# Optimization experiments

Measured on AMD Instinct MI355X. Metric: run time of the kernel, lower is better.

## Reference

```python
import jax, jax.numpy as jnp
import numpy as np

B, T, D = 4, 4096, 1024
H = 16
DH = D // H
F = 4096
EPS = 1e-5


def _layernorm(x, gamma, beta):
    mu = jnp.mean(x, axis=-1, keepdims=True)
    var = jnp.var(x, axis=-1, keepdims=True)
    return (x - mu) * jax.lax.rsqrt(var + EPS) * gamma + beta


def setup_inputs() -> dict:
    key = jax.random.key(0)
    ks = jax.random.split(key, 10)
    s = 0.02
    return {
        "x": jax.random.normal(ks[0], (B, T, D), dtype=jnp.float32),
        "Wqkv": jax.random.normal(ks[1], (D, 3 * D), dtype=jnp.float32) * s,
        "bqkv": jnp.zeros((3 * D,), dtype=jnp.float32),
        "Wo": jax.random.normal(ks[2], (D, D), dtype=jnp.float32) * s,
        "bo": jnp.zeros((D,), dtype=jnp.float32),
        "W1": jax.random.normal(ks[3], (D, F), dtype=jnp.float32) * s,
        "b1": jnp.zeros((F,), dtype=jnp.float32),
        "W2": jax.random.normal(ks[4], (F, D), dtype=jnp.float32) * s,
        "b2": jnp.zeros((D,), dtype=jnp.float32),
        "g1": jnp.ones((D,), dtype=jnp.float32),
        "be1": jnp.zeros((D,), dtype=jnp.float32),
        "g2": jnp.ones((D,), dtype=jnp.float32),
        "be2": jnp.zeros((D,), dtype=jnp.float32),
    }


def reference(x, Wqkv, bqkv, Wo, bo, W1, b1, W2, b2, g1, be1, g2, be2):
    # fused QKV projection: [B,T,3D]
    qkv = jnp.einsum("btd,de->bte", x, Wqkv) + bqkv
    q, k, v = jnp.split(qkv, 3, axis=-1)
    # [B,H,T,DH]
    q = q.reshape(B, T, H, DH).transpose(0, 2, 1, 3)
    k = k.reshape(B, T, H, DH).transpose(0, 2, 1, 3)
    v = v.reshape(B, T, H, DH).transpose(0, 2, 1, 3)
    scores = jnp.einsum("bhqd,bhkd->bhqk", q, k) / jnp.sqrt(jnp.float32(DH))
    attn = jax.nn.softmax(scores, axis=-1)
    ctx = jnp.einsum("bhqk,bhkd->bhqd", attn, v)
    ctx = ctx.transpose(0, 2, 1, 3).reshape(B, T, D)
    # output projection + residual + post-LN
    x = _layernorm(x + (jnp.einsum("btd,de->bte", ctx, Wo) + bo), g1, be1)
    # FFN (exact GELU, torch default) + residual + post-LN
    h = jax.nn.gelu(jnp.einsum("btd,df->btf", x, W1) + b1, approximate=False)
    ffn = jnp.einsum("btf,fd->btd", h, W2) + b2
    return _layernorm(x + ffn, g2, be2)
```

## Files before the change

### kernel.cpp

```cpp
#include <hip/hip_runtime.h>
#include <math.h>

typedef unsigned short u16;
typedef unsigned int   u32;
typedef __attribute__((ext_vector_type(8))) short short8;
typedef __attribute__((ext_vector_type(4))) float f32x4;

#define B_  4
#define T_  4096
#define D_  1024
#define H_  16
#define DH_ 64
#define F_  4096
#define EPS_ 1e-5f
#define QKV_LD (3 * D_)

#define QSCALE_ 0.18033688011112042f

__device__ __forceinline__ float b2f(u16 v) {
    union { u32 u; float f; } x; x.u = ((u32)v) << 16; return x.f;
}
__device__ __forceinline__ u16 f2b(float f) {
    union { u32 u; float f; } x; x.f = f;
    u32 r = (x.u >> 16) & 1u;
    return (u16)((x.u + 0x7fffu + r) >> 16);
}

__device__ __forceinline__ float ex2(float x) {
    float r;
    asm("v_exp_f32 %0, %1" : "=v"(r) : "v"(x));
    return r;
}
__device__ __forceinline__ float rcp_(float x) {
    float r;
    asm("v_rcp_f32 %0, %1" : "=v"(r) : "v"(x));
    return r;
}
__device__ __forceinline__ u32 cvtpk(float lo, float hi) {
    u32 r;
    asm("v_cvt_pk_bf16_f32 %0, %1, %2" : "=v"(r) : "v"(lo), "v"(hi));
    return r;
}
template<int CTRL>
__device__ __forceinline__ u32 dppu(u32 v) {
    return (u32)__builtin_amdgcn_update_dpp(0, (int)v, CTRL, 0xF, 0xF, true);
}

__device__ __forceinline__ float gelu_erf(float x) {
    const float z = fabsf(x) * 0.70710678118654752f;
    const float t = rcp_(1.0f + 0.3275911f * z);
    float poly = 1.061405429f;
    poly = poly * t - 1.453152027f;
    poly = poly * t + 1.421413741f;
    poly = poly * t - 0.284496736f;
    poly = poly * t + 0.254829592f;
    poly = poly * t;
    const float e = ex2(-z * z * 1.4426950408889634f);
    const float erfz = 1.0f - poly * e;
    const float se = copysignf(erfz, x);
    return 0.5f * x * (1.0f + se);
}

__device__ __forceinline__ void gll16(const u16* g, u16* ldsbase) {
    __builtin_amdgcn_global_load_lds(
        (const __attribute__((address_space(1))) void*)g,
        (__attribute__((address_space(3))) void*)ldsbase, 16, 0, 0);
}

__global__ __launch_bounds__(256) void conv_bf16_kernel(
    const float* __restrict__ in, u16* __restrict__ out)
{
    const int i = blockIdx.x * 256 + threadIdx.x;
    float4 v = ((const float4*)in)[i];
    ushort4 o;
    o.x = f2b(v.x); o.y = f2b(v.y); o.z = f2b(v.z); o.w = f2b(v.w);
    ((ushort4*)out)[i] = o;
}

__global__ __launch_bounds__(256) void transpose_bf16_kernel(
    const float* __restrict__ W, u16* __restrict__ Wt, int R, int C)
{
    __shared__ float tile[32][33];
    const int bx = blockIdx.x * 32;
    const int by = blockIdx.y * 32;
    const int tx = threadIdx.x & 31, ty = threadIdx.x >> 5;
#pragma unroll
    for (int p = 0; p < 4; ++p)
        tile[ty + p * 8][tx] = W[(size_t)(by + ty + p * 8) * C + bx + tx];
    __syncthreads();
#pragma unroll
    for (int p = 0; p < 4; ++p)
        Wt[(size_t)(bx + ty + p * 8) * R + by + tx] = f2b(tile[tx][ty + p * 8]);
}

template<bool CBF, int KU>
__global__ __launch_bounds__(256) void mfma_gemm(
    const u16* __restrict__ A, int lda,
    const u16* __restrict__ Bt, int ldbt,
    const float* __restrict__ bias,
    void* __restrict__ Cv, int ldc,
    int K, int act, int acc, int qcols)
{
    __shared__ __align__(16) u16 Al[KU][128 * 32];
    __shared__ __align__(16) u16 Bl[KU][128 * 32];

    const int tid  = threadIdx.x;
    const int lane = tid & 63, wave = tid >> 6;
    const int quad = lane >> 4, l16 = lane & 15;

    const int gx = gridDim.x;
    const int nwg = gx * gridDim.y;
    const int lin = blockIdx.y * gx + blockIdx.x;
    const int wg  = (lin & 7) * (nwg >> 3) + (lin >> 3);
    const int m0 = (wg / gx) * 128, n0 = (wg % gx) * 128;

    const int wm = (wave >> 1) * 64, wn = (wave & 1) * 64;

    int srow[2], sgk[2];
#pragma unroll
    for (int t = 0; t < 2; ++t) {
        const int c = wave * 128 + t * 64 + lane;
        srow[t] = c >> 2;
        sgk[t] = ((c & 3) ^ ((srow[t] >> 1) & 3)) * 8;
    }
    const u16* Ag = A  + (size_t)m0 * lda;
    const u16* Bg = Bt + (size_t)n0 * ldbt;
    const int apos = (quad ^ ((l16 >> 1) & 3)) * 8;

    f32x4 accr[4][4];
#pragma unroll
    for (int i = 0; i < 4; ++i)
#pragma unroll
        for (int j = 0; j < 4; ++j)
            accr[i][j] = (f32x4)(0.0f);

    for (int k0 = 0; k0 < K; k0 += 32 * KU) {
        __syncthreads();
#pragma unroll
        for (int h = 0; h < KU; ++h)
#pragma unroll
            for (int t = 0; t < 2; ++t) {
                gll16(Ag + (size_t)srow[t] * lda  + k0 + h * 32 + sgk[t],
                      &Al[h][(wave * 128 + t * 64) * 8]);
                gll16(Bg + (size_t)srow[t] * ldbt + k0 + h * 32 + sgk[t],
                      &Bl[h][(wave * 128 + t * 64) * 8]);
            }
        __syncthreads();

#pragma unroll
        for (int h = 0; h < KU; ++h) {
            short8 af[4], bf[4];
#pragma unroll
            for (int i = 0; i < 4; ++i)
                af[i] = *(const short8*)&Al[h][(wm + i * 16 + l16) * 32 + apos];
#pragma unroll
            for (int j = 0; j < 4; ++j)
                bf[j] = *(const short8*)&Bl[h][(wn + j * 16 + l16) * 32 + apos];
#pragma unroll
            for (int i = 0; i < 4; ++i)
#pragma unroll
                for (int j = 0; j < 4; ++j)
                    accr[i][j] = __builtin_amdgcn_mfma_f32_16x16x32_bf16(
                        af[i], bf[j], accr[i][j], 0, 0, 0);
        }
    }

#pragma unroll
    for (int j = 0; j < 4; ++j) {
        const int cc = n0 + wn + j * 16 + l16;
        float bv = acc ? 0.0f : bias[cc];
        const float sc = (cc < qcols) ? QSCALE_ : 1.0f;
#pragma unroll
        for (int i = 0; i < 4; ++i) {
#pragma unroll
            for (int r = 0; r < 4; ++r) {
                const int rr = m0 + wm + i * 16 + quad * 4 + r;
                float v = (accr[i][j][r] + bv) * sc;
                if (act == 1)
                    v = gelu_erf(v);
                if (CBF) {
                    ((u16*)Cv)[(size_t)rr * ldc + cc] = f2b(v);
                } else {
                    float* dst = (float*)Cv + (size_t)rr * ldc + cc;
                    if (acc) v += *dst;
                    *dst = v;
                }
            }
        }
    }
}

__global__ __launch_bounds__(256) void attn_mfma_kernel(
    const u16* __restrict__ qkv, u16* __restrict__ ctx)
{
    __shared__ u16 Ks[64 * 72];
    __shared__ u16 Vt[64 * 72];
    __shared__ u16 Ps[4][32 * 72];

    const int tid  = threadIdx.x;
    const int lane = tid & 63, wave = tid >> 6;
    const int quad = lane >> 4, l16 = lane & 15;
    const int odd  = l16 & 1;

    const int gx = gridDim.x, gy = gridDim.y;
    const int nwg = gx * gy * gridDim.z;
    const int lin = (blockIdx.z * gy + blockIdx.y) * gx + blockIdx.x;
    const int wg  = (lin & 7) * (nwg >> 3) + (lin >> 3);
    const int q0 = (wg % gx) * 128;
    const int h  = (wg / gx) % gy;
    const int b  = wg / (gx * gy);

    short8 ones8;
#pragma unroll
    for (int i = 0; i < 8; ++i) ones8[i] = (short)0x3F80;

    short8 aq[2][2];
    {
        const u16* qb = qkv + (size_t)(b * T_ + q0 + wave * 32) * QKV_LD + h * DH_;
#pragma unroll
        for (int u = 0; u < 2; ++u)
#pragma unroll
            for (int s = 0; s < 2; ++s)
                aq[u][s] = *(const short8*)(qb + (size_t)(u * 16 + l16) * QKV_LD + s * 32 + quad * 8);
    }

    const int srow = tid >> 3;
    const int scol = (tid & 7) * 8;
    const int odd8 = srow & 1;
    const u16* kg = qkv + (size_t)(b * T_) * QKV_LD + D_     + h * DH_;
    const u16* vg = qkv + (size_t)(b * T_) * QKV_LD + 2 * D_ + h * DH_;

    short8 kreg[2], vreg[2];
#pragma unroll
    for (int half = 0; half < 2; ++half) {
        const int row = srow + half * 32;
        kreg[half] = *(const short8*)(kg + (size_t)row * QKV_LD + scol);
        vreg[half] = *(const short8*)(vg + (size_t)row * QKV_LD + scol);
    }

    f32x4 o_acc[2][4];
#pragma unroll
    for (int u = 0; u < 2; ++u)
#pragma unroll
        for (int nt = 0; nt < 4; ++nt)
            o_acc[u][nt] = (f32x4)(0.0f);
    f32x4 l_acc[2];
    l_acc[0] = (f32x4)(0.0f);
    l_acc[1] = (f32x4)(0.0f);

    for (int kt = 0; kt < T_; kt += 64) {
        __syncthreads();
#pragma unroll
        for (int half = 0; half < 2; ++half) {
            const int row = srow + half * 32;
            *(short8*)&Ks[row * 72 + scol] = kreg[half];

            union { short8 s; u32 w[4]; } vv;
            vv.s = vreg[half];
            const u32 ws0 = dppu<0x118>(vv.w[0]);
            const u32 ws1 = dppu<0x118>(vv.w[1]);
            const u32 sl2 = dppu<0x108>(vv.w[2]);
            const u32 sl3 = dppu<0x108>(vv.w[3]);
            const int rowb = row & ~1;
            const int koff = rowb ^ scol;
#pragma unroll
            for (int J = 0; J < 4; ++J) {
                const u32 wj   = vv.w[J >> 1];
                const u32 wj4  = vv.w[2 + (J >> 1)];
                const u32 wsj  = (J >> 1) ? ws1 : ws0;
                const u32 slj4 = (J >> 1) ? sl3 : sl2;
                const u32 selfJ  = (J & 1) ? (wj   >> 16) : (wj   & 0xFFFFu);
                const u32 selfJ4 = (J & 1) ? (wj4  >> 16) : (wj4  & 0xFFFFu);
                const u32 nbrJ   = (J & 1) ? (wsj  >> 16) : (wsj  & 0xFFFFu);
                const u32 nbrJ4  = (J & 1) ? (slj4 >> 16) : (slj4 & 0xFFFFu);
                const u32 lo16 = odd8 ? nbrJ4  : selfJ;
                const u32 hi16 = odd8 ? selfJ4 : nbrJ;
                const int dh = scol + J + (odd8 ? 4 : 0);
                *(u32*)&Vt[dh * 72 + koff] = lo16 | (hi16 << 16);
            }
        }
        __syncthreads();

        if (kt + 64 < T_) {
#pragma unroll
            for (int half = 0; half < 2; ++half) {
                const int row = srow + half * 32;
                kreg[half] = *(const short8*)(kg + (size_t)(kt + 64 + row) * QKV_LD + scol);
                vreg[half] = *(const short8*)(vg + (size_t)(kt + 64 + row) * QKV_LD + scol);
            }
        }

        f32x4 sa[2][4];
#pragma unroll
        for (int u = 0; u < 2; ++u)
#pragma unroll
            for (int nt = 0; nt < 4; ++nt)
                sa[u][nt] = (f32x4)(0.0f);
        __builtin_amdgcn_s_setprio(1);
#pragma unroll
        for (int s = 0; s < 2; ++s) {
            short8 kb[4];
#pragma unroll
            for (int nt = 0; nt < 4; ++nt)
                kb[nt] = *(const short8*)&Ks[(nt * 16 + l16) * 72 + s * 32 + quad * 8];
#pragma unroll
            for (int u = 0; u < 2; ++u)
#pragma unroll
                for (int nt = 0; nt < 4; ++nt)
                    sa[u][nt] = __builtin_amdgcn_mfma_f32_16x16x32_bf16(
                        aq[u][s], kb[nt], sa[u][nt], 0, 0, 0);
        }
        __builtin_amdgcn_s_setprio(0);

#pragma unroll
        for (int u = 0; u < 2; ++u) {
#pragma unroll
            for (int nt = 0; nt < 4; ++nt) {
                float p[4];
#pragma unroll
                for (int r = 0; r < 4; ++r)
                    p[r] = ex2(sa[u][nt][r]);
#pragma unroll
                for (int g = 0; g < 2; ++g) {
                    union { float f; u32 u; } a0, a1, b0, b1;
                    a0.f = p[2 * g];
                    a1.f = p[2 * g + 1];
                    b0.u = dppu<0x111>(a0.u);
                    b1.u = dppu<0x101>(a1.u);
                    const float lo = odd ? b1.f : a0.f;
                    const float hi = odd ? a1.f : b0.f;
                    *(u32*)&Ps[wave][(u * 16 + quad * 4 + 2 * g + odd) * 72
                                     + nt * 16 + l16 - odd] = cvtpk(lo, hi);
                }
            }
        }

        __builtin_amdgcn_s_setprio(1);
#pragma unroll
        for (int s = 0; s < 2; ++s) {
            short8 pa[2];
#pragma unroll
            for (int u = 0; u < 2; ++u)
                pa[u] = *(const short8*)&Ps[wave][(u * 16 + l16) * 72 + s * 32 + quad * 8];
#pragma unroll
            for (int u = 0; u < 2; ++u)
                l_acc[u] = __builtin_amdgcn_mfma_f32_16x16x32_bf16(
                    pa[u], ones8, l_acc[u], 0, 0, 0);
#pragma unroll
            for (int nt = 0; nt < 4; ++nt) {
                const int dh = nt * 16 + l16;
                short8 vb = *(const short8*)&Vt[dh * 72 + ((s * 32 + quad * 8) ^ (dh & 56))];
#pragma unroll
                for (int u = 0; u < 2; ++u)
                    o_acc[u][nt] = __builtin_amdgcn_mfma_f32_16x16x32_bf16(
                        pa[u], vb, o_acc[u][nt], 0, 0, 0);
            }
        }
        __builtin_amdgcn_s_setprio(0);
    }

#pragma unroll
    for (int u = 0; u < 2; ++u) {
#pragma unroll
        for (int r = 0; r < 4; ++r) {
            const float inv = 1.0f / l_acc[u][r];
            const size_t row = (size_t)(b * T_ + q0 + wave * 32 + u * 16 + quad * 4 + r);
#pragma unroll
            for (int nt = 0; nt < 4; ++nt)
                ctx[row * D_ + h * DH_ + nt * 16 + l16] = f2b(o_acc[u][nt][r] * inv);
        }
    }
}

template<bool ABF, bool BBF, bool OBF>
__global__ __launch_bounds__(256) void add_ln_kernel(
    const void* __restrict__ av, const void* __restrict__ bv,
    const float* __restrict__ g, const float* __restrict__ be,
    void* __restrict__ outv)
{
    const int row = blockIdx.x;
    const int tid = threadIdx.x;

    float v[4];
    if (ABF) {
        ushort4 va = *(const ushort4*)((const u16*)av + (size_t)row * D_ + tid * 4);
        v[0] = b2f(va.x); v[1] = b2f(va.y); v[2] = b2f(va.z); v[3] = b2f(va.w);
    } else {
        float4 va = *(const float4*)((const float*)av + (size_t)row * D_ + tid * 4);
        v[0] = va.x; v[1] = va.y; v[2] = va.z; v[3] = va.w;
    }
    if (BBF) {
        ushort4 vb = *(const ushort4*)((const u16*)bv + (size_t)row * D_ + tid * 4);
        v[0] += b2f(vb.x); v[1] += b2f(vb.y); v[2] += b2f(vb.z); v[3] += b2f(vb.w);
    } else {
        float4 vb = *(const float4*)((const float*)bv + (size_t)row * D_ + tid * 4);
        v[0] += vb.x; v[1] += vb.y; v[2] += vb.z; v[3] += vb.w;
    }

    float s  = v[0] + v[1] + v[2] + v[3];
    float ss = v[0]*v[0] + v[1]*v[1] + v[2]*v[2] + v[3]*v[3];
#pragma unroll
    for (int off = 32; off > 0; off >>= 1) {
        s  += __shfl_down(s,  off, 64);
        ss += __shfl_down(ss, off, 64);
    }
    __shared__ float ws[4], wss[4], stats[2];
    const int wave = tid >> 6, lane = tid & 63;
    if (lane == 0) { ws[wave] = s; wss[wave] = ss; }
    __syncthreads();
    if (tid == 0) {
        float ts  = ws[0] + ws[1] + ws[2] + ws[3];
        float tss = wss[0] + wss[1] + wss[2] + wss[3];
        float mu  = ts * (1.0f / D_);
        float var = tss * (1.0f / D_) - mu * mu;
        stats[0] = mu;
        stats[1] = rsqrtf(var + EPS_);
    }
    __syncthreads();
    const float mu = stats[0], rs = stats[1];

    const float4 g4  = *(const float4*)(g  + tid * 4);
    const float4 be4 = *(const float4*)(be + tid * 4);
    float gg[4]  = {g4.x, g4.y, g4.z, g4.w};
    float beb[4] = {be4.x, be4.y, be4.z, be4.w};
    if (OBF) {
        ushort4 o;
        o.x = f2b((v[0] - mu) * rs * gg[0] + beb[0]);
        o.y = f2b((v[1] - mu) * rs * gg[1] + beb[1]);
        o.z = f2b((v[2] - mu) * rs * gg[2] + beb[2]);
        o.w = f2b((v[3] - mu) * rs * gg[3] + beb[3]);
        *(ushort4*)((u16*)outv + (size_t)row * D_ + tid * 4) = o;
    } else {
        float4 o;
        o.x = (v[0] - mu) * rs * gg[0] + beb[0];
        o.y = (v[1] - mu) * rs * gg[1] + beb[1];
        o.z = (v[2] - mu) * rs * gg[2] + beb[2];
        o.w = (v[3] - mu) * rs * gg[3] + beb[3];
        *(float4*)((float*)outv + (size_t)row * D_ + tid * 4) = o;
    }
}

extern "C" void kernel_launch(void* const* d_in, const int* in_sizes, int n_in,
                              void* d_out, int out_size, void* d_ws, size_t ws_size,
                              hipStream_t stream)
{
    const float* x    = (const float*)d_in[0];
    const float* Wqkv = (const float*)d_in[1];
    const float* bqkv = (const float*)d_in[2];
    const float* Wo   = (const float*)d_in[3];
    const float* bo   = (const float*)d_in[4];
    const float* W1   = (const float*)d_in[5];
    const float* b1   = (const float*)d_in[6];
    const float* W2   = (const float*)d_in[7];
    const float* b2   = (const float*)d_in[8];
    const float* g1   = (const float*)d_in[9];
    const float* be1  = (const float*)d_in[10];
    const float* g2   = (const float*)d_in[11];
    const float* be2  = (const float*)d_in[12];
    float* out = (float*)d_out;

    const int M = B_ * T_;
    char* ws = (char*)d_ws;
    char* sc = (char*)d_out;

    u16*   qkvB   = (u16*)ws;
    u16*   ctxB   = (u16*)(ws + (size_t)100663296);
    float* proj   = (float*)ws;
    u16*   x1B    = (u16*)(ws + (size_t)100663296);
    u16*   hchunk = (u16*)ws;
    u16*   ffnB   = (u16*)(ws + (size_t)67108864);

    u16* xB    = (u16*)sc;
    u16* WqkvT = (u16*)(sc + (size_t)33554432);
    u16* WoT   = (u16*)(sc + (size_t)39845888);
    u16* W1T   = (u16*)(sc + (size_t)41943040);
    u16* W2T   = (u16*)(sc + (size_t)50331648);

    dim3 blk(256);

    conv_bf16_kernel<<<dim3(M * D_ / 1024), blk, 0, stream>>>(x, xB);
    transpose_bf16_kernel<<<dim3(3 * D_ / 32, D_ / 32), blk, 0, stream>>>(Wqkv, WqkvT, D_, 3 * D_);
    transpose_bf16_kernel<<<dim3(D_ / 32, D_ / 32), blk, 0, stream>>>(Wo, WoT, D_, D_);
    transpose_bf16_kernel<<<dim3(F_ / 32, D_ / 32), blk, 0, stream>>>(W1, W1T, D_, F_);
    transpose_bf16_kernel<<<dim3(D_ / 32, F_ / 32), blk, 0, stream>>>(W2, W2T, F_, D_);

    mfma_gemm<true, 1><<<dim3(3 * D_ / 128, M / 128), blk, 0, stream>>>(
        xB, D_, WqkvT, D_, bqkv, qkvB, 3 * D_, D_, 0, 0, D_);

    attn_mfma_kernel<<<dim3(T_ / 128, H_, B_), blk, 0, stream>>>(qkvB, ctxB);

    mfma_gemm<false, 1><<<dim3(D_ / 128, M / 128), blk, 0, stream>>>(
        ctxB, D_, WoT, D_, bo, proj, D_, D_, 0, 0, 0);

    add_ln_kernel<false, false, true><<<dim3(M), blk, 0, stream>>>(x, proj, g1, be1, x1B);

    for (int mc = 0; mc < 2; ++mc) {
        const size_t m0 = (size_t)mc * 8192;
        mfma_gemm<true, 1><<<dim3(F_ / 128, 8192 / 128), blk, 0, stream>>>(
            x1B + m0 * D_, D_, W1T, D_, b1, hchunk, F_, D_, 1, 0, 0);
        mfma_gemm<true, 2><<<dim3(D_ / 128, 8192 / 128), blk, 0, stream>>>(
            hchunk, F_, W2T, F_, b2, ffnB + m0 * D_, D_, F_, 0, 0, 0);
    }

    add_ln_kernel<true, true, false><<<dim3(M), blk, 0, stream>>>(x1B, ffnB, g2, be2, out);
}
```

Baseline: 1.080 ms.

## Keep attention probabilities in registers via transposed MFMA and bpermute

Swaps the MFMA operand order so S is computed transposed (keys × queries). The exponentiated probabilities can then feed the PV MFMA directly from registers, using ds_bpermute to exchange half-lane data, and the per-wave Ps shared-memory staging buffer is removed. The V-transpose LDS swizzle is changed to match the new read pattern. Output stores become packed 8-byte writes along head dimension, using a reciprocal intrinsic. This cuts LDS traffic and shared memory use, but adds cross-lane permutes and depends on getting the new swizzle exactly right.

```diff
diff --git a/kernel.cpp b/kernel.cpp
--- a/kernel.cpp
+++ b/kernel.cpp
@@ -195,12 +195,12 @@
 {
     __shared__ u16 Ks[64 * 72];
     __shared__ u16 Vt[64 * 72];
-    __shared__ u16 Ps[4][32 * 72];
 
     const int tid  = threadIdx.x;
     const int lane = tid & 63, wave = tid >> 6;
     const int quad = lane >> 4, l16 = lane & 15;
-    const int odd  = l16 & 1;
+    const bool hi  = lane >= 32;
+    const int bpa  = (lane ^ 32) << 2;
 
     const int gx = gridDim.x, gy = gridDim.y;
     const int nwg = gx * gy * gridDim.z;
@@ -262,7 +262,9 @@
             const u32 sl2 = dppu<0x108>(vv.w[2]);
             const u32 sl3 = dppu<0x108>(vv.w[3]);
             const int rowb = row & ~1;
-            const int koff = rowb ^ scol;
+            const int sw = ((rowb & ~12) | ((rowb & 4) << 1) | ((rowb & 8) >> 1))
+                           ^ ((rowb & 16) >> 2);
+            const int koff = sw ^ scol;
 #pragma unroll
             for (int J = 0; J < 4; ++J) {
                 const u32 wj   = vv.w[J >> 1];
@@ -308,52 +310,44 @@
 #pragma unroll
                 for (int nt = 0; nt < 4; ++nt)
                     sa[u][nt] = __builtin_amdgcn_mfma_f32_16x16x32_bf16(
-                        aq[u][s], kb[nt], sa[u][nt], 0, 0, 0);
+                        kb[nt], aq[u][s], sa[u][nt], 0, 0, 0);
         }
         __builtin_amdgcn_s_setprio(0);
 
-#pragma unroll
-        for (int u = 0; u < 2; ++u) {
-#pragma unroll
-            for (int nt = 0; nt < 4; ++nt) {
-                float p[4];
-#pragma unroll
-                for (int r = 0; r < 4; ++r)
-                    p[r] = ex2(sa[u][nt][r]);
-#pragma unroll
-                for (int g = 0; g < 2; ++g) {
-                    union { float f; u32 u; } a0, a1, b0, b1;
-                    a0.f = p[2 * g];
-                    a1.f = p[2 * g + 1];
-                    b0.u = dppu<0x111>(a0.u);
-                    b1.u = dppu<0x101>(a1.u);
-                    const float lo = odd ? b1.f : a0.f;
-                    const float hi = odd ? a1.f : b0.f;
-                    *(u32*)&Ps[wave][(u * 16 + quad * 4 + 2 * g + odd) * 72
-                                     + nt * 16 + l16 - odd] = cvtpk(lo, hi);
-                }
-            }
-        }
+        u32 pk[2][4][2];
+#pragma unroll
+        for (int u = 0; u < 2; ++u)
+#pragma unroll
+            for (int nt = 0; nt < 4; ++nt)
+#pragma unroll
+                for (int w = 0; w < 2; ++w)
+                    pk[u][nt][w] = cvtpk(ex2(sa[u][nt][2 * w]),
+                                         ex2(sa[u][nt][2 * w + 1]));
 
         __builtin_amdgcn_s_setprio(1);
 #pragma unroll
         for (int s = 0; s < 2; ++s) {
-            short8 pa[2];
-#pragma unroll
-            for (int u = 0; u < 2; ++u)
-                pa[u] = *(const short8*)&Ps[wave][(u * 16 + l16) * 72 + s * 32 + quad * 8];
-#pragma unroll
-            for (int u = 0; u < 2; ++u)
-                l_acc[u] = __builtin_amdgcn_mfma_f32_16x16x32_bf16(
-                    pa[u], ones8, l_acc[u], 0, 0, 0);
+            short8 vb[4];
 #pragma unroll
             for (int nt = 0; nt < 4; ++nt) {
                 const int dh = nt * 16 + l16;
-                short8 vb = *(const short8*)&Vt[dh * 72 + ((s * 32 + quad * 8) ^ (dh & 56))];
-#pragma unroll
-                for (int u = 0; u < 2; ++u)
+                vb[nt] = *(const short8*)&Vt[dh * 72 + ((s * 32 + quad * 8) ^ (dh & 56))];
+            }
+#pragma unroll
+            for (int u = 0; u < 2; ++u) {
+                union { u32 w[4]; short8 v; } pb;
+                pb.w[0] = hi ? pk[u][2 * s + 1][0] : pk[u][2 * s][0];
+                pb.w[1] = hi ? pk[u][2 * s + 1][1] : pk[u][2 * s][1];
+                const u32 c0 = hi ? pk[u][2 * s][0] : pk[u][2 * s + 1][0];
+                const u32 c1 = hi ? pk[u][2 * s][1] : pk[u][2 * s + 1][1];
+                pb.w[2] = (u32)__builtin_amdgcn_ds_bpermute(bpa, (int)c0);
+                pb.w[3] = (u32)__builtin_amdgcn_ds_bpermute(bpa, (int)c1);
+                l_acc[u] = __builtin_amdgcn_mfma_f32_16x16x32_bf16(
+                    ones8, pb.v, l_acc[u], 0, 0, 0);
+#pragma unroll
+                for (int nt = 0; nt < 4; ++nt)
                     o_acc[u][nt] = __builtin_amdgcn_mfma_f32_16x16x32_bf16(
-                        pa[u], vb, o_acc[u][nt], 0, 0, 0);
+                        vb[nt], pb.v, o_acc[u][nt], 0, 0, 0);
             }
         }
         __builtin_amdgcn_s_setprio(0);
@@ -361,13 +355,14 @@
 
 #pragma unroll
     for (int u = 0; u < 2; ++u) {
-#pragma unroll
-        for (int r = 0; r < 4; ++r) {
-            const float inv = 1.0f / l_acc[u][r];
-            const size_t row = (size_t)(b * T_ + q0 + wave * 32 + u * 16 + quad * 4 + r);
-#pragma unroll
-            for (int nt = 0; nt < 4; ++nt)
-                ctx[row * D_ + h * DH_ + nt * 16 + l16] = f2b(o_acc[u][nt][r] * inv);
+        const float inv = rcp_(l_acc[u][0]);
+        const size_t qrow = (size_t)(b * T_ + q0 + wave * 32 + u * 16 + l16);
+#pragma unroll
+        for (int nt = 0; nt < 4; ++nt) {
+            uint2 o;
+            o.x = cvtpk(o_acc[u][nt][0] * inv, o_acc[u][nt][1] * inv);
+            o.y = cvtpk(o_acc[u][nt][2] * inv, o_acc[u][nt][3] * inv);
+            *(uint2*)&ctx[qrow * D_ + h * DH_ + nt * 16 + quad * 4] = o;
         }
     }
 }
```

New measurement: 1.025 ms (median of 2 runs). 5.1% less time.
